# Kernel tuning notes

Measured on AMD Instinct MI355X. Metric: run time of the kernel, lower is better.

The kernel has to match this reference:

```python
import jax, jax.numpy as jnp
import numpy as np

N_NODES = 100000
D_FEAT = 128
N_EDGES = 1600000


def setup_inputs() -> dict:
    key = jax.random.key(0)
    k1, k2, k3 = jax.random.split(key, 3)
    x = jax.random.normal(k1, (N_NODES, D_FEAT), dtype=jnp.float32)
    edge_weight = jax.random.uniform(k2, (N_EDGES,), dtype=jnp.float32)
    edge_index = jax.random.randint(k3, (2, N_EDGES), 0, N_NODES, dtype=jnp.int64)
    return {"x": x, "edge_weight": edge_weight, "edge_index": edge_index, "n_nodes": N_NODES}


def reference(x, edge_weight, edge_index, n_nodes):
    # h_v = sum_{(u->v) in E} w_uv * h_u  (gather -> scale -> scatter_add)
    src = edge_index[0]
    dst = edge_index[1]
    msg = x[src] * edge_weight[:, None]          # (E, d)
    out = jax.ops.segment_sum(msg, dst, num_segments=n_nodes)  # (N, d)
    return out
```

## Files before the change

### kernel.cpp

```cpp
#include <hip/hip_runtime.h>


constexpr int D_FEAT = 128;
constexpr int NPB = 128;
constexpr int NBK_MAX = 1024;
constexpr int HBLK = 256;
constexpr int CTILE = 3136;
constexpr int CAP = 3072;

typedef float v4f __attribute__((ext_vector_type(4)));

__global__ __launch_bounds__(256) void scatter_atomic_kernel(
    const float* __restrict__ x, const float* __restrict__ w,
    const int* __restrict__ src_idx, const int* __restrict__ dst_idx,
    float* __restrict__ out, int n_edges) {
  long long tid = (long long)blockIdx.x * blockDim.x + threadIdx.x;
  int lane = (int)(tid & 31);
  long long e = tid >> 5;
  if (e >= n_edges) return;
  int s = src_idx[e];
  int d = dst_idx[e];
  float wt = w[e];
  float4 v = ((const float4*)(x + (size_t)s * D_FEAT))[lane];
  float* o = out + (size_t)d * D_FEAT + (size_t)lane * 4;
  atomicAdd(o + 0, v.x * wt);
  atomicAdd(o + 1, v.y * wt);
  atomicAdd(o + 2, v.z * wt);
  atomicAdd(o + 3, v.w * wt);
}

__device__ __forceinline__ int block_excl_scan(int v, int* sh, int* total) {
  const int lane = threadIdx.x & 63;
  const int wid = threadIdx.x >> 6;
  const int nw = blockDim.x >> 6;
  int inc = v;
  #pragma unroll
  for (int o = 1; o < 64; o <<= 1) {
    int t = __shfl_up(inc, o, 64);
    if (lane >= o) inc += t;
  }
  if (lane == 63) sh[wid] = inc;
  __syncthreads();
  if (threadIdx.x == 0) {
    int a = 0;
    for (int k = 0; k < nw; ++k) { int t = sh[k]; sh[k] = a; a += t; }
    sh[nw] = a;
  }
  __syncthreads();
  int r = sh[wid] + inc - v;
  if (total) *total = sh[nw];
  __syncthreads();
  return r;
}

__global__ __launch_bounds__(512) void hist_kernel(
    const int* __restrict__ dst, int* __restrict__ gtot,
    int* __restrict__ gcur, int* __restrict__ gbase, int* __restrict__ done,
    int n_edges, int nbk, int tile) {
  __shared__ int h[NBK_MAX];
  __shared__ int sh[9];
  __shared__ int slast;
  const int tid = threadIdx.x;
  const int b = blockIdx.x;
  for (int k = tid; k < nbk; k += 512) h[k] = 0;
  __syncthreads();
  int base = b * tile;
  int lim = min(base + tile, n_edges);
  for (int i = base + tid; i < lim; i += 512)
    atomicAdd(&h[((unsigned)dst[i]) >> 7], 1);
  __syncthreads();
  for (int k = tid; k < nbk; k += 512)
    if (h[k]) atomicAdd(&gtot[k], h[k]);
  __threadfence();
  __syncthreads();
  if (tid == 0)
    slast = (__hip_atomic_fetch_add(done, 1, __ATOMIC_ACQ_REL,
                                    __HIP_MEMORY_SCOPE_AGENT) ==
             (int)gridDim.x - 1);
  __syncthreads();
  if (slast) {
    int carry = 0;
    for (int kb = 0; kb < nbk; kb += 512) {
      int k = kb + tid;
      int v = (k < nbk)
                  ? __hip_atomic_load(&gtot[k], __ATOMIC_RELAXED,
                                      __HIP_MEMORY_SCOPE_AGENT)
                  : 0;
      int tot;
      int ex = block_excl_scan(v, sh, &tot);
      if (k < nbk) { gbase[k] = carry + ex; gcur[k] = carry + ex; }
      carry += tot;
    }
    if (tid == 0) gbase[nbk] = carry;
  }
}

__global__ __launch_bounds__(512) void scatter_kernel(
    const int* __restrict__ src, const int* __restrict__ dst,
    const float* __restrict__ w, int* __restrict__ gcur,
    uint2* __restrict__ csr, int n_edges, int nbk, int tile) {
  __shared__ uint2 ed[CTILE];
  __shared__ unsigned short bkt[CTILE];
  __shared__ unsigned int prm[CTILE];
  __shared__ int h[NBK_MAX];
  __shared__ int lb[NBK_MAX];
  __shared__ int cur[NBK_MAX];
  __shared__ int gb[NBK_MAX];
  __shared__ int sh[9];

  const int tid = threadIdx.x;
  const int b = blockIdx.x;
  int base = b * tile;
  int lim = min(base + tile, n_edges);
  int cnt = max(lim - base, 0);

  for (int k = tid; k < nbk; k += 512) { h[k] = 0; cur[k] = 0; }
  __syncthreads();
  for (int i = base + tid; i < lim; i += 512) {
    int j = i - base;
    unsigned d = (unsigned)dst[i];
    unsigned k = d >> 7;
    ed[j] = make_uint2((unsigned)src[i] | ((d & 127u) << 20),
                       __float_as_uint(w[i]));
    bkt[j] = (unsigned short)k;
    atomicAdd(&h[k], 1);
  }
  __syncthreads();
  {
    int carry = 0;
    for (int kb = 0; kb < nbk; kb += 512) {
      int k = kb + tid;
      int v = (k < nbk) ? h[k] : 0;
      int tot;
      int ex = block_excl_scan(v, sh, &tot);
      if (k < nbk) {
        lb[k] = carry + ex;
        if (v) gb[k] = atomicAdd(&gcur[k], v);
      }
      carry += tot;
    }
  }
  __syncthreads();
  for (int j = tid; j < cnt; j += 512) {
    int k = bkt[j];
    int oc = atomicAdd(&cur[k], 1);
    prm[lb[k] + oc] = (unsigned)j | ((unsigned)k << 12);
  }
  __syncthreads();
  for (int p = tid; p < cnt; p += 512) {
    unsigned v = prm[p];
    int j = (int)(v & 0xFFFu);
    int k = (int)(v >> 12);
    csr[gb[k] + (p - lb[k])] = ed[j];
  }
}

__global__ __launch_bounds__(256) void gather_kernel(
    const float* __restrict__ x, const int* __restrict__ gbase,
    const uint2* __restrict__ csr, float* __restrict__ out, int n_nodes) {
  __shared__ uint2 eds[CAP];
  __shared__ unsigned short perm[CAP];
  __shared__ int loff[NPB + 1];
  __shared__ int lcur[NPB];
  __shared__ int sh[9];

  const int b = blockIdx.x;
  const int tid = threadIdx.x;
  const int beg = gbase[b];
  const int end = gbase[b + 1];
  const int cnt = end - beg;
  const int nbase = b * NPB;

  const int wv = tid >> 6;
  const int lane = tid & 63;
  const int f = lane & 31;
  const int half = lane >> 5;
  const float4* X = (const float4*)x;

  if (cnt <= CAP) {
    if (tid < NPB) lcur[tid] = 0;
    __syncthreads();
    for (int i = tid; i < cnt; i += 256) {
      uint2 e = csr[beg + i];
      eds[i] = e;
      atomicAdd(&lcur[e.x >> 20], 1);
    }
    __syncthreads();
    {
      int v = (tid < NPB) ? lcur[tid] : 0;
      int ex = block_excl_scan(v, sh, nullptr);
      __syncthreads();
      if (tid < NPB) { loff[tid] = ex; lcur[tid] = 0; }
      if (tid == 0) loff[NPB] = cnt;
    }
    __syncthreads();
    for (int i = tid; i < cnt; i += 256) {
      int dl = eds[i].x >> 20;
      int pos = loff[dl] + atomicAdd(&lcur[dl], 1);
      perm[pos] = (unsigned short)i;
    }
    __syncthreads();

    for (int n = wv; n < NPB; n += 4) {
      int node = nbase + n;
      if (node >= n_nodes) break;
      int jb = loff[n];
      int je = loff[n + 1];
      float4 a0 = make_float4(0.f, 0.f, 0.f, 0.f);
      float4 a1 = make_float4(0.f, 0.f, 0.f, 0.f);
      float4 a2 = make_float4(0.f, 0.f, 0.f, 0.f);
      float4 a3 = make_float4(0.f, 0.f, 0.f, 0.f);
      int j = jb + half;
      for (; j + 6 < je; j += 8) {
        uint2 e0 = eds[perm[j]];
        uint2 e1 = eds[perm[j + 2]];
        uint2 e2 = eds[perm[j + 4]];
        uint2 e3 = eds[perm[j + 6]];
        float4 v0 = X[(size_t)(e0.x & 0xFFFFFu) * 32 + f];
        float4 v1 = X[(size_t)(e1.x & 0xFFFFFu) * 32 + f];
        float4 v2 = X[(size_t)(e2.x & 0xFFFFFu) * 32 + f];
        float4 v3 = X[(size_t)(e3.x & 0xFFFFFu) * 32 + f];
        float w0 = __uint_as_float(e0.y);
        float w1 = __uint_as_float(e1.y);
        float w2 = __uint_as_float(e2.y);
        float w3 = __uint_as_float(e3.y);
        a0.x += w0 * v0.x; a0.y += w0 * v0.y; a0.z += w0 * v0.z; a0.w += w0 * v0.w;
        a1.x += w1 * v1.x; a1.y += w1 * v1.y; a1.z += w1 * v1.z; a1.w += w1 * v1.w;
        a2.x += w2 * v2.x; a2.y += w2 * v2.y; a2.z += w2 * v2.z; a2.w += w2 * v2.w;
        a3.x += w3 * v3.x; a3.y += w3 * v3.y; a3.z += w3 * v3.z; a3.w += w3 * v3.w;
      }
      for (; j < je; j += 2) {
        uint2 e0 = eds[perm[j]];
        float4 v0 = X[(size_t)(e0.x & 0xFFFFFu) * 32 + f];
        float w0 = __uint_as_float(e0.y);
        a0.x += w0 * v0.x; a0.y += w0 * v0.y; a0.z += w0 * v0.z; a0.w += w0 * v0.w;
      }
      a0.x += a1.x + a2.x + a3.x;
      a0.y += a1.y + a2.y + a3.y;
      a0.z += a1.z + a2.z + a3.z;
      a0.w += a1.w + a2.w + a3.w;
      a0.x += __shfl_xor(a0.x, 32, 64);
      a0.y += __shfl_xor(a0.y, 32, 64);
      a0.z += __shfl_xor(a0.z, 32, 64);
      a0.w += __shfl_xor(a0.w, 32, 64);
      if (half == 0) {
        v4f val = {a0.x, a0.y, a0.z, a0.w};
        __builtin_nontemporal_store(val, (v4f*)out + (size_t)node * 32 + f);
      }
    }
  } else {
    for (int n = wv; n < NPB; n += 4) {
      int node = nbase + n;
      if (node >= n_nodes) break;
      float4 a0 = make_float4(0.f, 0.f, 0.f, 0.f);
      for (int j = half; j < cnt; j += 2) {
        uint2 e = csr[beg + j];
        if ((int)(e.x >> 20) == n) {
          float4 v = X[(size_t)(e.x & 0xFFFFFu) * 32 + f];
          float wt = __uint_as_float(e.y);
          a0.x += wt * v.x; a0.y += wt * v.y; a0.z += wt * v.z; a0.w += wt * v.w;
        }
      }
      a0.x += __shfl_xor(a0.x, 32, 64);
      a0.y += __shfl_xor(a0.y, 32, 64);
      a0.z += __shfl_xor(a0.z, 32, 64);
      a0.w += __shfl_xor(a0.w, 32, 64);
      if (half == 0) {
        v4f val = {a0.x, a0.y, a0.z, a0.w};
        __builtin_nontemporal_store(val, (v4f*)out + (size_t)node * 32 + f);
      }
    }
  }
}

extern "C" void kernel_launch(void* const* d_in, const int* in_sizes, int n_in,
                              void* d_out, int out_size, void* d_ws, size_t ws_size,
                              hipStream_t stream) {
  const float* x  = (const float*)d_in[0];
  const float* w  = (const float*)d_in[1];
  const int* eidx = (const int*)d_in[2];

  int n_edges = in_sizes[1];
  int n_nodes = out_size / D_FEAT;
  const int* src = eidx;
  const int* dst = eidx + n_edges;
  float* out = (float*)d_out;

  const int nbk = (n_nodes + NPB - 1) / NPB;
  const int htile = (n_edges + HBLK - 1) / HBLK;
  const int cblk = (n_edges + CTILE - 11 - 1) / (CTILE - 11);
  const int ctile = cblk > 0 ? (n_edges + cblk - 1) / cblk : 0;

  const size_t ctrl_ints = 1024 + 1024 + 4 + 1028;
  size_t need = ctrl_ints * 4 + (size_t)n_edges * 8;
  if (n_edges <= 0) {
    hipMemsetAsync(d_out, 0, (size_t)out_size * sizeof(float), stream);
    return;
  }
  if (ws_size < need || nbk > NBK_MAX || n_nodes >= (1 << 20) ||
      ctile > CTILE) {
    hipMemsetAsync(d_out, 0, (size_t)out_size * sizeof(float), stream);
    long long total_threads = (long long)n_edges * 32;
    long long grid = (total_threads + 255) / 256;
    scatter_atomic_kernel<<<(dim3)(unsigned)grid, 256, 0, stream>>>(
        x, w, src, dst, out, n_edges);
    return;
  }

  int* gtot = (int*)d_ws;
  int* gcur = gtot + 1024;
  int* done = gcur + 1024;
  int* gbase = done + 4;
  uint2* csr = (uint2*)(gbase + 1028);

  hipMemsetAsync(gtot, 0, (1024 + 1024 + 4) * sizeof(int), stream);

  hist_kernel<<<HBLK, 512, 0, stream>>>(dst, gtot, gcur, gbase, done,
                                        n_edges, nbk, htile);
  scatter_kernel<<<cblk, 512, 0, stream>>>(src, dst, w, gcur, csr,
                                           n_edges, nbk, ctile);
  gather_kernel<<<nbk, 256, 0, stream>>>(x, gbase, csr, out, n_nodes);
}
```

Before: 279.6 us.

## Replace histogram-scan bucketing with fixed-capacity segments and direct scatter

Each 64-node bucket gets a fixed-capacity slot region in the workspace sized from the mean plus a statistical margin. This removes the global histogram and scan pass: an init kernel seeds the per-bucket cursors, and the scatter kernel builds a per-block histogram, reserves ranges atomically, and writes edges straight to global memory without staging them in LDS. Halving NPB gives the gather more blocks, each with a smaller LDS footprint. In exchange the CSR writes are no longer coalesced, and a bucket that overflows its capacity falls back to a full scan of all edges.

```diff
diff --git a/kernel.cpp b/kernel.cpp
--- a/kernel.cpp
+++ b/kernel.cpp
@@ -1,12 +1,14 @@
 #include <hip/hip_runtime.h>
+#include <math.h>
 
 
 constexpr int D_FEAT = 128;
-constexpr int NPB = 128;
-constexpr int NBK_MAX = 1024;
+constexpr int NPB = 64;
+constexpr int LOG_NPB = 6;
+constexpr int NBK_MAX = 2048;
 constexpr int HBLK = 256;
-constexpr int CTILE = 3136;
-constexpr int CAP = 3072;
+constexpr int SCB = 256;
+constexpr int CAP = 1536;
 
 typedef float v4f __attribute__((ext_vector_type(4)));
 
@@ -67,7 +69,7 @@
   int base = b * tile;
   int lim = min(base + tile, n_edges);
   for (int i = base + tid; i < lim; i += 512)
-    atomicAdd(&h[((unsigned)dst[i]) >> 7], 1);
+    atomicAdd(&h[((unsigned)dst[i]) >> LOG_NPB], 1);
   __syncthreads();
   for (int k = tid; k < nbk; k += 512)
     if (h[k]) atomicAdd(&gtot[k], h[k]);
@@ -95,69 +97,50 @@
   }
 }
 
+__global__ __launch_bounds__(256) void init_seg_kernel(int* __restrict__ gcur,
+                                                       int nbk, int capb) {
+  int k = blockIdx.x * 256 + threadIdx.x;
+  if (k < nbk) gcur[k] = k * capb;
+}
+
 __global__ __launch_bounds__(512) void scatter_kernel(
     const int* __restrict__ src, const int* __restrict__ dst,
     const float* __restrict__ w, int* __restrict__ gcur,
-    uint2* __restrict__ csr, int n_edges, int nbk, int tile) {
-  __shared__ uint2 ed[CTILE];
-  __shared__ unsigned short bkt[CTILE];
-  __shared__ unsigned int prm[CTILE];
+    uint2* __restrict__ csr, int n_edges, int nbk, int tile, int capb) {
   __shared__ int h[NBK_MAX];
-  __shared__ int lb[NBK_MAX];
   __shared__ int cur[NBK_MAX];
   __shared__ int gb[NBK_MAX];
-  __shared__ int sh[9];
-
   const int tid = threadIdx.x;
   const int b = blockIdx.x;
   int base = b * tile;
   int lim = min(base + tile, n_edges);
-  int cnt = max(lim - base, 0);
-
-  for (int k = tid; k < nbk; k += 512) { h[k] = 0; cur[k] = 0; }
+  for (int k = tid; k < nbk; k += 512) h[k] = 0;
+  __syncthreads();
+  for (int i = base + tid; i < lim; i += 512)
+    atomicAdd(&h[((unsigned)dst[i]) >> LOG_NPB], 1);
+  __syncthreads();
+  for (int k = tid; k < nbk; k += 512) {
+    cur[k] = 0;
+    int v = h[k];
+    if (v) gb[k] = atomicAdd(&gcur[k], v);
+  }
   __syncthreads();
   for (int i = base + tid; i < lim; i += 512) {
-    int j = i - base;
     unsigned d = (unsigned)dst[i];
-    unsigned k = d >> 7;
-    ed[j] = make_uint2((unsigned)src[i] | ((d & 127u) << 20),
-                       __float_as_uint(w[i]));
-    bkt[j] = (unsigned short)k;
-    atomicAdd(&h[k], 1);
-  }
-  __syncthreads();
-  {
-    int carry = 0;
-    for (int kb = 0; kb < nbk; kb += 512) {
-      int k = kb + tid;
-      int v = (k < nbk) ? h[k] : 0;
-      int tot;
-      int ex = block_excl_scan(v, sh, &tot);
-      if (k < nbk) {
-        lb[k] = carry + ex;
-        if (v) gb[k] = atomicAdd(&gcur[k], v);
-      }
-      carry += tot;
-    }
-  }
-  __syncthreads();
-  for (int j = tid; j < cnt; j += 512) {
-    int k = bkt[j];
-    int oc = atomicAdd(&cur[k], 1);
-    prm[lb[k] + oc] = (unsigned)j | ((unsigned)k << 12);
-  }
-  __syncthreads();
-  for (int p = tid; p < cnt; p += 512) {
-    unsigned v = prm[p];
-    int j = (int)(v & 0xFFFu);
-    int k = (int)(v >> 12);
-    csr[gb[k] + (p - lb[k])] = ed[j];
+    unsigned k = d >> LOG_NPB;
+    int pos = gb[k] + atomicAdd(&cur[k], 1);
+    if (capb == 0 || pos < (int)(k + 1) * capb)
+      csr[pos] = make_uint2((unsigned)src[i] | ((d & (NPB - 1u)) << 20),
+                            __float_as_uint(w[i]));
   }
 }
 
 __global__ __launch_bounds__(256) void gather_kernel(
     const float* __restrict__ x, const int* __restrict__ gbase,
-    const uint2* __restrict__ csr, float* __restrict__ out, int n_nodes) {
+    const int* __restrict__ gcur, const uint2* __restrict__ csr,
+    float* __restrict__ out, int n_nodes, int capb,
+    const int* __restrict__ src, const int* __restrict__ dst,
+    const float* __restrict__ w, int n_edges) {
   __shared__ uint2 eds[CAP];
   __shared__ unsigned short perm[CAP];
   __shared__ int loff[NPB + 1];
@@ -166,9 +149,9 @@
 
   const int b = blockIdx.x;
   const int tid = threadIdx.x;
-  const int beg = gbase[b];
-  const int end = gbase[b + 1];
-  const int cnt = end - beg;
+  const int beg = capb ? b * capb : gbase[b];
+  const int cnt = gcur[b] - beg;
+  const int limcap = capb ? capb : CAP;
   const int nbase = b * NPB;
 
   const int wv = tid >> 6;
@@ -177,7 +160,7 @@
   const int half = lane >> 5;
   const float4* X = (const float4*)x;
 
-  if (cnt <= CAP) {
+  if (cnt <= limcap) {
     if (tid < NPB) lcur[tid] = 0;
     __syncthreads();
     for (int i = tid; i < cnt; i += 256) {
@@ -253,11 +236,10 @@
       int node = nbase + n;
       if (node >= n_nodes) break;
       float4 a0 = make_float4(0.f, 0.f, 0.f, 0.f);
-      for (int j = half; j < cnt; j += 2) {
-        uint2 e = csr[beg + j];
-        if ((int)(e.x >> 20) == n) {
-          float4 v = X[(size_t)(e.x & 0xFFFFFu) * 32 + f];
-          float wt = __uint_as_float(e.y);
+      for (int j = half; j < n_edges; j += 2) {
+        if (dst[j] == node) {
+          float4 v = X[(size_t)src[j] * 32 + f];
+          float wt = w[j];
           a0.x += wt * v.x; a0.y += wt * v.y; a0.z += wt * v.z; a0.w += wt * v.w;
         }
       }
@@ -286,19 +268,32 @@
   const int* dst = eidx + n_edges;
   float* out = (float*)d_out;
 
-  const int nbk = (n_nodes + NPB - 1) / NPB;
-  const int htile = (n_edges + HBLK - 1) / HBLK;
-  const int cblk = (n_edges + CTILE - 11 - 1) / (CTILE - 11);
-  const int ctile = cblk > 0 ? (n_edges + cblk - 1) / cblk : 0;
-
-  const size_t ctrl_ints = 1024 + 1024 + 4 + 1028;
-  size_t need = ctrl_ints * 4 + (size_t)n_edges * 8;
   if (n_edges <= 0) {
     hipMemsetAsync(d_out, 0, (size_t)out_size * sizeof(float), stream);
     return;
   }
-  if (ws_size < need || nbk > NBK_MAX || n_nodes >= (1 << 20) ||
-      ctile > CTILE) {
+
+  const int nbk = (n_nodes + NPB - 1) / NPB;
+  const int stile = (n_edges + SCB - 1) / SCB;
+  const int htile = (n_edges + HBLK - 1) / HBLK;
+
+  const size_t ctrl_ints = (size_t)NBK_MAX + NBK_MAX + 4 + (NBK_MAX + 4);
+  const size_t ctrl_bytes = ctrl_ints * 4;
+  long long slots_avail =
+      ((long long)ws_size - (long long)ctrl_bytes) / 8;
+
+  long long mean = n_edges / (nbk > 0 ? nbk : 1);
+  int capb_min = (int)(mean + 7.0 * sqrt((double)(mean > 0 ? mean : 1)) + 32);
+  int capb = 0;
+  if (nbk > 0 && slots_avail > 0) {
+    long long c = slots_avail / nbk;
+    if (c > CAP) c = CAP;
+    capb = (int)(c & ~7LL);
+  }
+  bool seg_ok = (capb >= capb_min);
+  bool exact_ok = (slots_avail >= (long long)n_edges);
+
+  if ((!seg_ok && !exact_ok) || nbk > NBK_MAX || n_nodes >= (1 << 20)) {
     hipMemsetAsync(d_out, 0, (size_t)out_size * sizeof(float), stream);
     long long total_threads = (long long)n_edges * 32;
     long long grid = (total_threads + 255) / 256;
@@ -308,16 +303,24 @@
   }
 
   int* gtot = (int*)d_ws;
-  int* gcur = gtot + 1024;
-  int* done = gcur + 1024;
+  int* gcur = gtot + NBK_MAX;
+  int* done = gcur + NBK_MAX;
   int* gbase = done + 4;
-  uint2* csr = (uint2*)(gbase + 1028);
-
-  hipMemsetAsync(gtot, 0, (1024 + 1024 + 4) * sizeof(int), stream);
-
-  hist_kernel<<<HBLK, 512, 0, stream>>>(dst, gtot, gcur, gbase, done,
-                                        n_edges, nbk, htile);
-  scatter_kernel<<<cblk, 512, 0, stream>>>(src, dst, w, gcur, csr,
-                                           n_edges, nbk, ctile);
-  gather_kernel<<<nbk, 256, 0, stream>>>(x, gbase, csr, out, n_nodes);
-}
+  uint2* csr = (uint2*)(gbase + NBK_MAX + 4);
+
+  if (seg_ok) {
+    init_seg_kernel<<<(nbk + 255) / 256, 256, 0, stream>>>(gcur, nbk, capb);
+    scatter_kernel<<<SCB, 512, 0, stream>>>(src, dst, w, gcur, csr,
+                                            n_edges, nbk, stile, capb);
+    gather_kernel<<<nbk, 256, 0, stream>>>(x, gbase, gcur, csr, out, n_nodes,
+                                           capb, src, dst, w, n_edges);
+  } else {
+    hipMemsetAsync(gtot, 0, (size_t)(NBK_MAX * 2 + 4) * sizeof(int), stream);
+    hist_kernel<<<HBLK, 512, 0, stream>>>(dst, gtot, gcur, gbase, done,
+                                          n_edges, nbk, htile);
+    scatter_kernel<<<SCB, 512, 0, stream>>>(src, dst, w, gcur, csr,
+                                            n_edges, nbk, stile, 0);
+    gather_kernel<<<nbk, 256, 0, stream>>>(x, gbase, gcur, csr, out, n_nodes,
+                                           0, src, dst, w, n_edges);
+  }
+}
```

New measurement: 254.3 us. -9.1%, faster.
